# Kernel tuning notes

Hardware: AMD Instinct MI355X
Metric: run time of the kernel (lower is better)

The kernel has to match this reference:

```python
import jax, jax.numpy as jnp
import numpy as np

HEADS = 6
EPS = 1e-5


def _na_idx(L, k, d):
    # NATTEN-style dilated neighborhood: work within dilation cosets,
    # clamp window to stay inside the image (window shifts at borders).
    i = np.arange(L)
    g = i % d
    p = i // d
    Lg = (L - g + d - 1) // d  # coset length per position
    start = np.clip(p - k // 2, 0, Lg - k)
    j = np.arange(k)
    nbr = g[:, None] + d * (start[:, None] + j[None, :])          # [L,k] neighbor coords
    rel = (start[:, None] + j[None, :]) - p[:, None] + (k - 1)    # [L,k] rpb index in [0,2k-2]
    return jnp.asarray(nbr, jnp.int32), jnp.asarray(rel, jnp.int32)


def _na2d(x, qkv_w, qkv_b, proj_w, proj_b, rpb, heads, k, d):
    # x: [B,H,W,C] NHWC neighborhood attention with relative positional bias
    B, H, W, C = x.shape
    dh = C // heads
    scale = dh ** -0.5
    qkv = (x @ qkv_w + qkv_b).reshape(B, H, W, 3, heads, dh)
    qkv = jnp.transpose(qkv, (3, 0, 4, 1, 2, 5))  # [3,B,h,H,W,dh]
    q, kk, v = qkv[0] * scale, qkv[1], qkv[2]
    nh, rh = _na_idx(H, k, d)
    nw, rw = _na_idx(W, k, d)

    def gather(t):  # [B,h,H,W,dh] -> [B,h,H,W,k,k,dh]
        t = t[:, :, nh]              # [B,h,H,k,W,dh]
        t = t[:, :, :, :, nw]        # [B,h,H,k,W,k,dh]
        return jnp.transpose(t, (0, 1, 2, 4, 3, 5, 6))

    kn, vn = gather(kk), gather(v)
    attn = jnp.einsum('bhxyd,bhxyijd->bhxyij', q, kn)  # [B,h,H,W,k,k]
    bias = rpb[:, rh]                  # [h,H,k,2k-1]
    bias = bias[:, :, :, rw]           # [h,H,k,W,k]
    bias = jnp.transpose(bias, (0, 1, 3, 2, 4))  # [h,H,W,k,k]
    attn = attn + bias[None]
    attn = jax.nn.softmax(attn.reshape(B, heads, H, W, k * k), axis=-1)
    attn = attn.reshape(B, heads, H, W, k, k)
    out = jnp.einsum('bhxyij,bhxyijd->bhxyd', attn, vn)
    out = jnp.transpose(out, (0, 2, 3, 1, 4)).reshape(B, H, W, C)
    return out @ proj_w + proj_b


def _rln(x, w, b, m1_w, m1_b, m2_w, m2_b):
    # Revised LayerNorm: normalize over (C,H,W) per sample; meta1/meta2 are 1x1 convs on std/mean
    mean = jnp.mean(x, axis=(1, 2, 3), keepdims=True)
    std = jnp.sqrt(jnp.mean((x - mean) ** 2, axis=(1, 2, 3), keepdims=True) + EPS)
    out = (x - mean) / std * w + b
    rescale = m1_w[None, :, None, None] * std + m1_b[None, :, None, None]
    rebias = m2_w[None, :, None, None] * mean + m2_b[None, :, None, None]
    return out, rescale, rebias


def _c11(x, w, b):  # 1x1 conv on NCHW == per-pixel linear
    return jnp.einsum('bchw,oc->bohw', x, w) + b[None, :, None, None]


def _gelu(x):
    return jax.nn.gelu(x, approximate=False)


def reference(x, ln_w, ln_b, m1_w, m1_b, m2_w, m2_b, qkv1_w, qkv1_b, proj1_w, proj1_b, rpb1, qkv2_w, qkv2_b, proj2_w, proj2_b, rpb2, mlp_w1, mlp_b1, mlp_w2, mlp_b2, bn_g, bn_b, bn_m, bn_v, pa_w1, pa_b1, pa_w2, pa_b2, ca_w1, ca_b1, ca_w2, ca_b2, m2a_w1, m2a_b1, m2a_w2, m2a_b2):
    # ---- NA block 1 (kernel 7, dilation 1) ----
    sc = x
    y, rs, rb = _rln(x, ln_w, ln_b, m1_w, m1_b, m2_w, m2_b)
    a = _na2d(jnp.transpose(y, (0, 2, 3, 1)), qkv1_w, qkv1_b, proj1_w, proj1_b, rpb1, HEADS, 7, 1)
    x = sc + jnp.transpose(a, (0, 3, 1, 2)) * rs + rb
    # ---- NA block 2 (kernel 5, dilation 8) ----
    sc = x
    y, rs, rb = _rln(x, ln_w, ln_b, m1_w, m1_b, m2_w, m2_b)
    a = _na2d(jnp.transpose(y, (0, 2, 3, 1)), qkv2_w, qkv2_b, proj2_w, proj2_b, rpb2, HEADS, 5, 8)
    x = sc + jnp.transpose(a, (0, 3, 1, 2)) * rs + rb
    # ---- MLP (source reuses the pre-attn2 shortcut `sc`) ----
    y, rs, rb = _rln(x, ln_w, ln_b, m1_w, m1_b, m2_w, m2_b)
    m = _c11(jax.nn.relu(_c11(y, mlp_w1, mlp_b1)), mlp_w2, mlp_b2)
    x = sc + m * rs + rb
    # ---- BN + pixel attention + channel attention + mlp2 ----
    sc = x
    inv = jax.lax.rsqrt(bn_v + EPS)
    y = (x - bn_m[None, :, None, None]) * (inv * bn_g)[None, :, None, None] + bn_b[None, :, None, None]
    pa = jax.nn.sigmoid(_c11(_gelu(_c11(y, pa_w1, pa_b1)), pa_w2, pa_b2))  # [B,1,H,W]
    y = pa * y
    gap = jnp.mean(y, axis=(2, 3), keepdims=True)
    ca = jax.nn.sigmoid(_c11(_gelu(_c11(gap, ca_w1, ca_b1)), ca_w2, ca_b2))  # [B,C,1,1]
    y = ca * y
    y = _c11(_gelu(_c11(y, m2a_w1, m2a_b1)), m2a_w2, m2a_b2)
    return sc + y


def setup_inputs() -> dict:
    key = jax.random.key(0)
    B, C, H, W, HID = 4, 96, 64, 64, 384
    ks = iter(jax.random.split(key, 48))

    def rn(shape, s=0.02):
        return jax.random.normal(next(ks), shape, jnp.float32) * s

    d = {}
    d['x'] = jax.random.normal(next(ks), (B, C, H, W), jnp.float32)
    d['ln_w'] = jnp.ones((1, C, 1, 1), jnp.float32)
    d['ln_b'] = jnp.zeros((1, C, 1, 1), jnp.float32)
    d['m1_w'] = rn((C,)); d['m1_b'] = jnp.ones((C,), jnp.float32)
    d['m2_w'] = rn((C,)); d['m2_b'] = jnp.zeros((C,), jnp.float32)
    d['qkv1_w'] = rn((C, 3 * C)); d['qkv1_b'] = jnp.zeros((3 * C,), jnp.float32)
    d['proj1_w'] = rn((C, C)); d['proj1_b'] = jnp.zeros((C,), jnp.float32)
    d['rpb1'] = rn((HEADS, 13, 13))
    d['qkv2_w'] = rn((C, 3 * C)); d['qkv2_b'] = jnp.zeros((3 * C,), jnp.float32)
    d['proj2_w'] = rn((C, C)); d['proj2_b'] = jnp.zeros((C,), jnp.float32)
    d['rpb2'] = rn((HEADS, 9, 9))
    d['mlp_w1'] = rn((HID, C)); d['mlp_b1'] = jnp.zeros((HID,), jnp.float32)
    d['mlp_w2'] = rn((C, HID)); d['mlp_b2'] = jnp.zeros((C,), jnp.float32)
    d['bn_g'] = jnp.ones((C,), jnp.float32); d['bn_b'] = jnp.zeros((C,), jnp.float32)
    d['bn_m'] = jnp.zeros((C,), jnp.float32); d['bn_v'] = jnp.ones((C,), jnp.float32)
    d['pa_w1'] = rn((C // 8, C)); d['pa_b1'] = jnp.zeros((C // 8,), jnp.float32)
    d['pa_w2'] = rn((1, C // 8)); d['pa_b2'] = jnp.zeros((1,), jnp.float32)
    d['ca_w1'] = rn((C, C)); d['ca_b1'] = jnp.zeros((C,), jnp.float32)
    d['ca_w2'] = rn((C, C)); d['ca_b2'] = jnp.zeros((C,), jnp.float32)
    d['m2a_w1'] = rn((C, C)); d['m2a_b1'] = jnp.zeros((C,), jnp.float32)
    d['m2a_w2'] = rn((C, C)); d['m2a_b2'] = jnp.zeros((C,), jnp.float32)
    return d
```

## Files before the change

kernel.cpp:

```cpp
#include <hip/hip_runtime.h>
#include <math.h>

#define CC 96
#define NP 4096
#define NHEADS 6
#define NELEMF 393216.0f
#define EPSF 1e-5f

typedef __attribute__((ext_vector_type(8))) short bf16x8;
typedef __attribute__((ext_vector_type(4))) float f32x4;
#define MFMA16(a,b,c) __builtin_amdgcn_mfma_f32_16x16x32_bf16(a,b,c,0,0,0)

#define WS_STATS 0
#define WQKV1  64
#define WQKV2  (WQKV1+13824)
#define WPROJ1 (WQKV2+13824)
#define WPROJ2 (WPROJ1+4608)
#define WMLP1  (WPROJ2+4608)
#define WMLP2  (WMLP1+18432)
#define WM2A1  (WMLP2+18432)
#define WM2A2  (WM2A1+4608)
#define WPA1T  (WM2A2+4608)
#define WBNS   (WPA1T+1152)
#define WS_YPM 84352
#define WS_Q   870784
#define WS_K   (WS_Q+1572864)
#define WS_V   (WS_K+1572864)
#define WS_ATTPM (WS_V+1572864)
#define WS_X1  (WS_ATTPM+786432)
#define WS_X2  (WS_X1+1572864)
#define WS_X3  (WS_X2+1572864)
#define WS_PA  (WS_X3+1572864)
#define WS_GAP (WS_PA+16384)
#define WS_CA  (WS_GAP+384)

__device__ __forceinline__ float gelu_f(float x){
  return 0.5f * x * (1.0f + erff(x * 0.7071067811865476f));
}
__device__ __forceinline__ float sigmoid_f(float x){
  return 1.0f / (1.0f + __expf(-x));
}
__device__ __forceinline__ unsigned short bfr(float f){
  unsigned int u = __float_as_uint(f);
  u += 0x7fffu + ((u >> 16) & 1u);
  return (unsigned short)(u >> 16);
}
__device__ __forceinline__ unsigned int bfpack(float a, float b){
  return (unsigned int)bfr(a) | ((unsigned int)bfr(b) << 16);
}
__device__ __forceinline__ void get_ms(const float* st, int b, float& mean, float& inv, float& stdv){
  float s = st[b], s2 = st[4+b];
  mean = s * (1.0f/NELEMF);
  float var = fmaxf(s2 * (1.0f/NELEMF) - mean*mean, 0.0f);
  stdv = sqrtf(var + EPSF);
  inv = 1.0f / stdv;
}

__global__ void stats_kernel(const float* __restrict__ src, float* __restrict__ st){
  int b = blockIdx.x / CC, c = blockIdx.x % CC;
  const float* p = src + (b*CC + c)*NP;
  float s = 0.f, s2 = 0.f;
  for(int i = threadIdx.x; i < NP; i += 256){ float v = p[i]; s += v; s2 = fmaf(v, v, s2); }
  for(int off = 32; off > 0; off >>= 1){ s += __shfl_down(s, off); s2 += __shfl_down(s2, off); }
  __shared__ float ls[8];
  int wid = threadIdx.x >> 6;
  if((threadIdx.x & 63) == 0){ ls[wid] = s; ls[4+wid] = s2; }
  __syncthreads();
  if(threadIdx.x == 0){
    atomicAdd(&st[b],   ls[0]+ls[1]+ls[2]+ls[3]);
    atomicAdd(&st[4+b], ls[4]+ls[5]+ls[6]+ls[7]);
  }
}

__global__ void prep_weights(const float* __restrict__ q1, const float* __restrict__ q2,
                             const float* __restrict__ p1, const float* __restrict__ p2,
                             const float* __restrict__ w1, const float* __restrict__ w2,
                             const float* __restrict__ a1, const float* __restrict__ a2,
                             const float* __restrict__ pw1,
                             const float* __restrict__ bg, const float* __restrict__ bb,
                             const float* __restrict__ bm, const float* __restrict__ bv,
                             float* __restrict__ ws){
  int gid = blockIdx.x*256 + threadIdx.x;
  if(gid < 27648){ int n = gid/96, c = gid%96; ((unsigned short*)(ws+WQKV1))[gid] = bfr(q1[c*288+n]); }
  else if(gid < 55296){ int g = gid-27648; int n = g/96, c = g%96; ((unsigned short*)(ws+WQKV2))[g] = bfr(q2[c*288+n]); }
  else if(gid < 64512){ int g = gid-55296; int n = g/96, c = g%96; ((unsigned short*)(ws+WPROJ1))[g] = bfr(p1[c*96+n]); }
  else if(gid < 73728){ int g = gid-64512; int n = g/96, c = g%96; ((unsigned short*)(ws+WPROJ2))[g] = bfr(p2[c*96+n]); }
  else if(gid < 110592){ int g = gid-73728; ((unsigned short*)(ws+WMLP1))[g] = bfr(w1[g]); }
  else if(gid < 147456){ int g = gid-110592; ((unsigned short*)(ws+WMLP2))[g] = bfr(w2[g]); }
  else if(gid < 156672){ int g = gid-147456; ((unsigned short*)(ws+WM2A1))[g] = bfr(a1[g]); }
  else if(gid < 165888){ int g = gid-156672; ((unsigned short*)(ws+WM2A2))[g] = bfr(a2[g]); }
  else if(gid < 167040){ int g = gid-165888; int c = g/12, h = g%12; ws[WPA1T + g] = pw1[h*96+c]; }
  else if(gid < 167136){ int c = gid-167040;
    float sc = rsqrtf(bv[c] + EPSF) * bg[c];
    ws[WBNS + c] = sc;
    ws[WBNS + 96 + c] = bb[c] - bm[c]*sc;
  }
}

__global__ void __launch_bounds__(256) ln_tr_kernel(
    const float* __restrict__ src, const float* __restrict__ st,
    const float* __restrict__ lnw, const float* __restrict__ lnb,
    unsigned int* __restrict__ dst){
  int px0 = blockIdx.x*64; int b = px0 >> 12; int pxl0 = px0 & 4095;
  float mean, inv, stdv; get_ms(st, b, mean, inv, stdv);
  __shared__ float T[96*67];
  for(int idx = threadIdx.x; idx < 96*64; idx += 256){
    int c = idx >> 6, p = idx & 63;
    float s = inv*lnw[c]; float o = lnb[c] - mean*s;
    T[c*67 + p] = fmaf(src[(b*96 + c)*NP + pxl0 + p], s, o);
  }
  __syncthreads();
  for(int idx = threadIdx.x; idx < 64*48; idx += 256){
    int row = idx/48, cd = idx%48;
    dst[(px0 + row)*48 + cd] = bfpack(T[(2*cd)*67 + row], T[(2*cd+1)*67 + row]);
  }
}

__global__ void __launch_bounds__(256) y3_tr_kernel(
    const float* __restrict__ x3, const float* __restrict__ bns,
    const float* __restrict__ pa, const float* __restrict__ ca,
    unsigned int* __restrict__ dst){
  int px0 = blockIdx.x*64; int b = px0 >> 12; int pxl0 = px0 & 4095;
  __shared__ float T[96*67];
  for(int idx = threadIdx.x; idx < 96*64; idx += 256){
    int c = idx >> 6, p = idx & 63;
    float v = fmaf(x3[(b*96 + c)*NP + pxl0 + p], bns[c], bns[96 + c]);
    T[c*67 + p] = v * ca[b*96 + c] * pa[px0 + p];
  }
  __syncthreads();
  for(int idx = threadIdx.x; idx < 64*48; idx += 256){
    int row = idx/48, cd = idx%48;
    dst[(px0 + row)*48 + cd] = bfpack(T[(2*cd)*67 + row], T[(2*cd+1)*67 + row]);
  }
}

template<int K>
__device__ __forceinline__ void mfma_tile(const unsigned short* __restrict__ A,
                                          const unsigned short* __restrict__ W,
                                          int m_base, int n_base, f32x4 acc[2][3]){
  int lane = threadIdx.x & 63;
  int ml = lane & 15, q = lane >> 4;
  const bf16x8* a0 = (const bf16x8*)(A + (size_t)(m_base + ml)*K + q*8);
  const bf16x8* a1 = (const bf16x8*)(A + (size_t)(m_base + 16 + ml)*K + q*8);
  const bf16x8* b0 = (const bf16x8*)(W + (n_base + ml)*K + q*8);
  const bf16x8* b1 = (const bf16x8*)(W + (n_base + 16 + ml)*K + q*8);
  const bf16x8* b2 = (const bf16x8*)(W + (n_base + 32 + ml)*K + q*8);
  #pragma unroll
  for(int ks = 0; ks < K/32; ++ks){
    bf16x8 av0 = a0[ks*4], av1 = a1[ks*4];
    bf16x8 bv0 = b0[ks*4], bv1 = b1[ks*4], bv2 = b2[ks*4];
    acc[0][0] = MFMA16(av0, bv0, acc[0][0]);
    acc[0][1] = MFMA16(av0, bv1, acc[0][1]);
    acc[0][2] = MFMA16(av0, bv2, acc[0][2]);
    acc[1][0] = MFMA16(av1, bv0, acc[1][0]);
    acc[1][1] = MFMA16(av1, bv1, acc[1][1]);
    acc[1][2] = MFMA16(av1, bv2, acc[1][2]);
  }
}

__global__ void __launch_bounds__(256) gemm_qkv_kernel(
    const unsigned short* __restrict__ ypm, const unsigned short* __restrict__ wT,
    const float* __restrict__ qb,
    float* __restrict__ qo, float* __restrict__ ko, float* __restrict__ vo){
  int w = threadIdx.x >> 6, lane = threadIdx.x & 63;
  int ml = lane & 15, q = lane >> 4;
  int m_base = blockIdx.x*128 + w*32;
  int n0 = blockIdx.y*48;
  f32x4 acc[2][3];
  f32x4 z = {0.f,0.f,0.f,0.f};
  #pragma unroll
  for(int f=0; f<2; ++f) for(int g=0; g<3; ++g) acc[f][g] = z;
  mfma_tile<96>(ypm, wT, m_base, n0, acc);
  #pragma unroll
  for(int g = 0; g < 3; ++g){
    int nfb = n0 + g*16;
    int t = nfb/96, head = (nfb%96) >> 4;
    float scale = (t == 0) ? 0.25f : 1.0f;
    float* dst = (t == 0) ? qo : (t == 1) ? ko : vo;
    float bias = qb[nfb + ml];
    #pragma unroll
    for(int f = 0; f < 2; ++f){
      #pragma unroll
      for(int r = 0; r < 4; ++r){
        int m = m_base + f*16 + q*4 + r;
        int b = m >> 12, pxl = m & 4095;
        dst[(((size_t)(b*NHEADS + head))*NP + pxl)*16 + ml] = (acc[f][g][r] + bias)*scale;
      }
    }
  }
}

__global__ void __launch_bounds__(256) gemm_proj_kernel(
    const unsigned short* __restrict__ attpm, const unsigned short* __restrict__ wT,
    const float* __restrict__ pb, const float* __restrict__ scx, const float* __restrict__ st,
    const float* __restrict__ m1w, const float* __restrict__ m1b,
    const float* __restrict__ m2w, const float* __restrict__ m2b,
    float* __restrict__ dst, float* __restrict__ st_out){
  int w = threadIdx.x >> 6, lane = threadIdx.x & 63;
  int ml = lane & 15, q = lane >> 4;
  int m_base = blockIdx.x*128 + w*32;
  int n0 = blockIdx.y*48;
  f32x4 acc[2][3];
  f32x4 z = {0.f,0.f,0.f,0.f};
  #pragma unroll
  for(int f=0; f<2; ++f) for(int g=0; g<3; ++g) acc[f][g] = z;
  mfma_tile<96>(attpm, wT, m_base, n0, acc);
  __shared__ float T[48*133];
  #pragma unroll
  for(int f = 0; f < 2; ++f)
    #pragma unroll
    for(int g = 0; g < 3; ++g)
      #pragma unroll
      for(int r = 0; r < 4; ++r)
        T[(g*16 + ml)*133 + w*32 + f*16 + q*4 + r] = acc[f][g][r];
  __syncthreads();
  int b = (blockIdx.x*128) >> 12, pxl0 = (blockIdx.x*128) & 4095;
  float mean, inv, stdv; get_ms(st, b, mean, inv, stdv);
  float s = 0.f, s2 = 0.f;
  for(int idx = threadIdx.x; idx < 48*128; idx += 256){
    int row = idx >> 7, px = idx & 127;
    int n = n0 + row;
    float rsf = fmaf(m1w[n], stdv, m1b[n]);
    float rbf = fmaf(m2w[n], mean, m2b[n]);
    int ad = (b*CC + n)*NP + pxl0 + px;
    float val = scx[ad] + (T[row*133 + px] + pb[n])*rsf + rbf;
    dst[ad] = val;
    s += val; s2 = fmaf(val, val, s2);
  }
  for(int off = 32; off > 0; off >>= 1){ s += __shfl_down(s, off); s2 += __shfl_down(s2, off); }
  __shared__ float ls[8];
  int wid = threadIdx.x >> 6;
  if((threadIdx.x & 63) == 0){ ls[wid] = s; ls[4+wid] = s2; }
  __syncthreads();
  if(threadIdx.x == 0){
    atomicAdd(&st_out[b],   ls[0]+ls[1]+ls[2]+ls[3]);
    atomicAdd(&st_out[4+b], ls[4]+ls[5]+ls[6]+ls[7]);
  }
}

__global__ void __launch_bounds__(256) gemm_mlp1_kernel(
    const unsigned short* __restrict__ ypm, const unsigned short* __restrict__ wT,
    const float* __restrict__ b1, unsigned short* __restrict__ hid){
  int w = threadIdx.x >> 6, lane = threadIdx.x & 63;
  int ml = lane & 15, q = lane >> 4;
  int m_base = blockIdx.x*128 + w*32;
  int n0 = blockIdx.y*48;
  f32x4 acc[2][3];
  f32x4 z = {0.f,0.f,0.f,0.f};
  #pragma unroll
  for(int f=0; f<2; ++f) for(int g=0; g<3; ++g) acc[f][g] = z;
  mfma_tile<96>(ypm, wT, m_base, n0, acc);
  #pragma unroll
  for(int g = 0; g < 3; ++g){
    int n = n0 + g*16 + ml;
    float bias = b1[n];
    #pragma unroll
    for(int f = 0; f < 2; ++f)
      #pragma unroll
      for(int r = 0; r < 4; ++r){
        int m = m_base + f*16 + q*4 + r;
        hid[(size_t)m*384 + n] = bfr(fmaxf(acc[f][g][r] + bias, 0.f));
      }
  }
}

__global__ void __launch_bounds__(256) gemm_mlp2_kernel(
    const unsigned short* __restrict__ hid, const unsigned short* __restrict__ wT,
    const float* __restrict__ b2, const float* __restrict__ scx, const float* __restrict__ st,
    const float* __restrict__ m1w, const float* __restrict__ m1b,
    const float* __restrict__ m2w, const float* __restrict__ m2b,
    float* __restrict__ dst){
  int w = threadIdx.x >> 6, lane = threadIdx.x & 63;
  int ml = lane & 15, q = lane >> 4;
  int m_base = blockIdx.x*128 + w*32;
  int n0 = blockIdx.y*48;
  f32x4 acc[2][3];
  f32x4 z = {0.f,0.f,0.f,0.f};
  #pragma unroll
  for(int f=0; f<2; ++f) for(int g=0; g<3; ++g) acc[f][g] = z;
  mfma_tile<384>(hid, wT, m_base, n0, acc);
  __shared__ float T[48*133];
  #pragma unroll
  for(int f = 0; f < 2; ++f)
    #pragma unroll
    for(int g = 0; g < 3; ++g)
      #pragma unroll
      for(int r = 0; r < 4; ++r)
        T[(g*16 + ml)*133 + w*32 + f*16 + q*4 + r] = acc[f][g][r];
  __syncthreads();
  int b = (blockIdx.x*128) >> 12, pxl0 = (blockIdx.x*128) & 4095;
  float mean, inv, stdv; get_ms(st, b, mean, inv, stdv);
  for(int idx = threadIdx.x; idx < 48*128; idx += 256){
    int row = idx >> 7, px = idx & 127;
    int n = n0 + row;
    float rsf = fmaf(m1w[n], stdv, m1b[n]);
    float rbf = fmaf(m2w[n], mean, m2b[n]);
    int ad = (b*CC + n)*NP + pxl0 + px;
    dst[ad] = scx[ad] + (T[row*133 + px] + b2[n])*rsf + rbf;
  }
}

__global__ void __launch_bounds__(256) gemm_m2a1_kernel(
    const unsigned short* __restrict__ y3pm, const unsigned short* __restrict__ wT,
    const float* __restrict__ b1, unsigned short* __restrict__ tpm){
  int w = threadIdx.x >> 6, lane = threadIdx.x & 63;
  int ml = lane & 15, q = lane >> 4;
  int m_base = blockIdx.x*128 + w*32;
  int n0 = blockIdx.y*48;
  f32x4 acc[2][3];
  f32x4 z = {0.f,0.f,0.f,0.f};
  #pragma unroll
  for(int f=0; f<2; ++f) for(int g=0; g<3; ++g) acc[f][g] = z;
  mfma_tile<96>(y3pm, wT, m_base, n0, acc);
  #pragma unroll
  for(int g = 0; g < 3; ++g){
    int n = n0 + g*16 + ml;
    float bias = b1[n];
    #pragma unroll
    for(int f = 0; f < 2; ++f)
      #pragma unroll
      for(int r = 0; r < 4; ++r){
        int m = m_base + f*16 + q*4 + r;
        tpm[(size_t)m*96 + n] = bfr(gelu_f(acc[f][g][r] + bias));
      }
  }
}

__global__ void __launch_bounds__(256) gemm_m2a2_kernel(
    const unsigned short* __restrict__ tpm, const unsigned short* __restrict__ wT,
    const float* __restrict__ b2, const float* __restrict__ scx, float* __restrict__ outp){
  int w = threadIdx.x >> 6, lane = threadIdx.x & 63;
  int ml = lane & 15, q = lane >> 4;
  int m_base = blockIdx.x*128 + w*32;
  int n0 = blockIdx.y*48;
  f32x4 acc[2][3];
  f32x4 z = {0.f,0.f,0.f,0.f};
  #pragma unroll
  for(int f=0; f<2; ++f) for(int g=0; g<3; ++g) acc[f][g] = z;
  mfma_tile<96>(tpm, wT, m_base, n0, acc);
  __shared__ float T[48*133];
  #pragma unroll
  for(int f = 0; f < 2; ++f)
    #pragma unroll
    for(int g = 0; g < 3; ++g)
      #pragma unroll
      for(int r = 0; r < 4; ++r)
        T[(g*16 + ml)*133 + w*32 + f*16 + q*4 + r] = acc[f][g][r];
  __syncthreads();
  int b = (blockIdx.x*128) >> 12, pxl0 = (blockIdx.x*128) & 4095;
  for(int idx = threadIdx.x; idx < 48*128; idx += 256){
    int row = idx >> 7, px = idx & 127;
    int n = n0 + row;
    int ad = (b*CC + n)*NP + pxl0 + px;
    outp[ad] = scx[ad] + T[row*133 + px] + b2[n];
  }
}

template<int K, int D, int RPB>
__global__ void __launch_bounds__(256) attn_kernel(
    const float* __restrict__ qb, const float* __restrict__ kb,
    const float* __restrict__ vb, const float* __restrict__ rpb,
    unsigned short* __restrict__ outp){
  int bh = blockIdx.x >> 6;
  int x = blockIdx.x & 63;
  int head = bh % NHEADS, b = bh / NHEADS;

  int gx = x % D, px = x / D;
  int Lgx = (64 - gx + D - 1) / D;
  int sx = min(max(px - K/2, 0), Lgx - K);

  __shared__ float sm[2*K*1024];
  float* kl = sm;
  float* vl = sm + K*1024;
  const float* kg = kb + (size_t)bh*NP*16;
  const float* vg = vb + (size_t)bh*NP*16;
  int tid = threadIdx.x;
  #pragma unroll
  for(int i = 0; i < K; ++i){
    int hh = gx + D*(sx + i);
    ((float4*)(kl + i*1024))[tid] = ((const float4*)(kg + hh*1024))[tid];
    ((float4*)(vl + i*1024))[tid] = ((const float4*)(vg + hh*1024))[tid];
  }
  __syncthreads();

  int pixoff = tid >> 2, t = tid & 3;
  int y = pixoff;
  int pix = x*64 + y;
  const float4 q = *(const float4*)(qb + ((size_t)bh*NP + pix)*16 + 4*t);

  int gy = y % D, py = y / D;
  int Lgy = (64 - gy + D - 1) / D;
  int sy = min(max(py - K/2, 0), Lgy - K);

  float sc[K*K];
  #pragma unroll
  for(int i = 0; i < K; ++i){
    #pragma unroll
    for(int j = 0; j < K; ++j){
      int ww = gy + D*(sy + j);
      float4 kv = *(const float4*)(kl + i*1024 + ww*16 + 4*t);
      float s = q.x*kv.x;
      s = fmaf(q.y, kv.y, s); s = fmaf(q.z, kv.z, s); s = fmaf(q.w, kv.w, s);
      sc[i*K + j] = s;
    }
  }
  float mx = -1e30f;
  #pragma unroll
  for(int i = 0; i < K; ++i){
    const float* brow = rpb + (head*RPB + (sx + i - px + (K-1)))*RPB + (sy - py + (K-1));
    #pragma unroll
    for(int j = 0; j < K; ++j){
      float s = sc[i*K + j];
      s += __shfl_xor(s, 1);
      s += __shfl_xor(s, 2);
      s += brow[j];
      sc[i*K + j] = s;
      mx = fmaxf(mx, s);
    }
  }
  float sum = 0.f;
  #pragma unroll
  for(int n = 0; n < K*K; ++n){ float e = __expf(sc[n] - mx); sc[n] = e; sum += e; }
  float rs = 1.0f / sum;
  float4 acc = {0,0,0,0};
  #pragma unroll
  for(int i = 0; i < K; ++i){
    #pragma unroll
    for(int j = 0; j < K; ++j){
      int ww = gy + D*(sy + j);
      float wgt = sc[i*K + j] * rs;
      float4 vv = *(const float4*)(vl + i*1024 + ww*16 + 4*t);
      acc.x = fmaf(wgt, vv.x, acc.x); acc.y = fmaf(wgt, vv.y, acc.y);
      acc.z = fmaf(wgt, vv.z, acc.z); acc.w = fmaf(wgt, vv.w, acc.w);
    }
  }
  ushort4 o4;
  o4.x = bfr(acc.x); o4.y = bfr(acc.y); o4.z = bfr(acc.z); o4.w = bfr(acc.w);
  *(ushort4*)(outp + ((size_t)(b*NP + pix))*96 + head*16 + 4*t) = o4;
}

__global__ void __launch_bounds__(64) pa_kernel(
    const float* __restrict__ x3, const float* __restrict__ bns,
    const float* __restrict__ w1t, const float* __restrict__ b1,
    const float* __restrict__ w2, const float* __restrict__ b2,
    float* __restrict__ pa){
  int pix = blockIdx.x*64 + threadIdx.x;
  int b = blockIdx.x >> 6;
  int p = pix & 4095;
  float acc[12];
  #pragma unroll
  for(int h = 0; h < 12; ++h) acc[h] = b1[h];
  #pragma unroll 4
  for(int c = 0; c < CC; ++c){
    float yv = fmaf(x3[(b*CC + c)*NP + p], bns[c], bns[96 + c]);
    #pragma unroll
    for(int h = 0; h < 12; ++h) acc[h] = fmaf(yv, w1t[c*12 + h], acc[h]);
  }
  float s = b2[0];
  #pragma unroll
  for(int h = 0; h < 12; ++h) s = fmaf(gelu_f(acc[h]), w2[h], s);
  pa[pix] = sigmoid_f(s);
}

__global__ void gap_kernel(const float* __restrict__ x3, const float* __restrict__ bns,
                           const float* __restrict__ pa, float* __restrict__ gap){
  int b = blockIdx.x / CC, c = blockIdx.x % CC;
  float scb = bns[c], shb = bns[96 + c];
  float s = 0.f;
  for(int i = threadIdx.x; i < NP; i += 256)
    s = fmaf(fmaf(x3[(b*CC + c)*NP + i], scb, shb), pa[b*NP + i], s);
  for(int off = 32; off > 0; off >>= 1) s += __shfl_down(s, off);
  __shared__ float ls[4];
  if((threadIdx.x & 63) == 0) ls[threadIdx.x >> 6] = s;
  __syncthreads();
  if(threadIdx.x == 0) gap[blockIdx.x] = (ls[0]+ls[1]+ls[2]+ls[3]) * (1.0f/4096.0f);
}

__global__ void ca_kernel(const float* __restrict__ gap, const float* __restrict__ w1,
                          const float* __restrict__ b1, const float* __restrict__ w2,
                          const float* __restrict__ b2, float* __restrict__ ca){
  int b = blockIdx.x; int o = threadIdx.x;
  __shared__ float g[96], t[96];
  if(o < 96) g[o] = gap[b*96 + o];
  __syncthreads();
  if(o < 96){
    float a = b1[o];
    for(int c = 0; c < 96; ++c) a = fmaf(g[c], w1[o*96 + c], a);
    t[o] = gelu_f(a);
  }
  __syncthreads();
  if(o < 96){
    float a = b2[o];
    for(int c = 0; c < 96; ++c) a = fmaf(t[c], w2[o*96 + c], a);
    ca[b*96 + o] = sigmoid_f(a);
  }
}

extern "C" void kernel_launch(void* const* d_in, const int* in_sizes, int n_in,
                              void* d_out, int out_size, void* d_ws, size_t ws_size,
                              hipStream_t stream){
  (void)in_sizes; (void)n_in; (void)out_size; (void)ws_size;
  const float* x     = (const float*)d_in[0];
  const float* lnw   = (const float*)d_in[1];
  const float* lnb   = (const float*)d_in[2];
  const float* m1w   = (const float*)d_in[3];
  const float* m1b   = (const float*)d_in[4];
  const float* m2w   = (const float*)d_in[5];
  const float* m2b   = (const float*)d_in[6];
  const float* qkv1w = (const float*)d_in[7];
  const float* qkv1b = (const float*)d_in[8];
  const float* proj1w= (const float*)d_in[9];
  const float* proj1b= (const float*)d_in[10];
  const float* rpb1  = (const float*)d_in[11];
  const float* qkv2w = (const float*)d_in[12];
  const float* qkv2b = (const float*)d_in[13];
  const float* proj2w= (const float*)d_in[14];
  const float* proj2b= (const float*)d_in[15];
  const float* rpb2  = (const float*)d_in[16];
  const float* mw1   = (const float*)d_in[17];
  const float* mb1   = (const float*)d_in[18];
  const float* mw2   = (const float*)d_in[19];
  const float* mb2   = (const float*)d_in[20];
  const float* bng   = (const float*)d_in[21];
  const float* bnb   = (const float*)d_in[22];
  const float* bnm   = (const float*)d_in[23];
  const float* bnv   = (const float*)d_in[24];
  const float* paw1  = (const float*)d_in[25];
  const float* pab1  = (const float*)d_in[26];
  const float* paw2  = (const float*)d_in[27];
  const float* pab2  = (const float*)d_in[28];
  const float* caw1  = (const float*)d_in[29];
  const float* cab1  = (const float*)d_in[30];
  const float* caw2  = (const float*)d_in[31];
  const float* cab2  = (const float*)d_in[32];
  const float* aw1   = (const float*)d_in[33];
  const float* ab1   = (const float*)d_in[34];
  const float* aw2   = (const float*)d_in[35];
  const float* ab2   = (const float*)d_in[36];

  float* ws  = (float*)d_ws;
  float* out = (float*)d_out;
  float* st0 = ws + WS_STATS;
  float* st1 = st0 + 8;
  float* st2 = st0 + 16;
  unsigned short* ypm   = (unsigned short*)(ws + WS_YPM);
  float* q   = ws + WS_Q;
  float* k   = ws + WS_K;
  float* v   = ws + WS_V;
  unsigned short* attpm = (unsigned short*)(ws + WS_ATTPM);
  unsigned short* hid   = (unsigned short*)(ws + WS_Q);
  unsigned short* tpm   = (unsigned short*)(ws + WS_Q);
  float* x1  = ws + WS_X1;
  float* x2  = ws + WS_X2;
  float* x3  = ws + WS_X3;
  float* pab = ws + WS_PA;
  float* gpb = ws + WS_GAP;
  float* cab = ws + WS_CA;
  float* bns = ws + WBNS;

  hipMemsetAsync(d_ws, 0, 64*sizeof(float), stream);
  prep_weights<<<653, 256, 0, stream>>>(qkv1w, qkv2w, proj1w, proj2w, mw1, mw2, aw1, aw2,
                                        paw1, bng, bnb, bnm, bnv, ws);

  stats_kernel<<<384, 256, 0, stream>>>(x, st0);
  ln_tr_kernel<<<256, 256, 0, stream>>>(x, st0, lnw, lnb, (unsigned int*)ypm);
  gemm_qkv_kernel<<<dim3(128,6), 256, 0, stream>>>(ypm, (unsigned short*)(ws+WQKV1), qkv1b, q, k, v);
  attn_kernel<7,1,13><<<1536, 256, 0, stream>>>(q, k, v, rpb1, attpm);
  gemm_proj_kernel<<<dim3(128,2), 256, 0, stream>>>(attpm, (unsigned short*)(ws+WPROJ1), proj1b,
                                                    x, st0, m1w, m1b, m2w, m2b, x1, st1);

  ln_tr_kernel<<<256, 256, 0, stream>>>(x1, st1, lnw, lnb, (unsigned int*)ypm);
  gemm_qkv_kernel<<<dim3(128,6), 256, 0, stream>>>(ypm, (unsigned short*)(ws+WQKV2), qkv2b, q, k, v);
  attn_kernel<5,8,9><<<1536, 256, 0, stream>>>(q, k, v, rpb2, attpm);
  gemm_proj_kernel<<<dim3(128,2), 256, 0, stream>>>(attpm, (unsigned short*)(ws+WPROJ2), proj2b,
                                                    x1, st1, m1w, m1b, m2w, m2b, x2, st2);

  ln_tr_kernel<<<256, 256, 0, stream>>>(x2, st2, lnw, lnb, (unsigned int*)ypm);
  gemm_mlp1_kernel<<<dim3(128,8), 256, 0, stream>>>(ypm, (unsigned short*)(ws+WMLP1), mb1, hid);
  gemm_mlp2_kernel<<<dim3(128,2), 256, 0, stream>>>(hid, (unsigned short*)(ws+WMLP2), mb2,
                                                    x1, st2, m1w, m1b, m2w, m2b, x3);

  pa_kernel<<<256, 64, 0, stream>>>(x3, bns, ws + WPA1T, pab1, paw2, pab2, pab);
  gap_kernel<<<384, 256, 0, stream>>>(x3, bns, pab, gpb);
  ca_kernel<<<4, 128, 0, stream>>>(gpb, caw1, cab1, caw2, cab2, cab);
  y3_tr_kernel<<<256, 256, 0, stream>>>(x3, bns, pab, cab, (unsigned int*)ypm);
  gemm_m2a1_kernel<<<dim3(128,2), 256, 0, stream>>>(ypm, (unsigned short*)(ws+WM2A1), ab1, tpm);
  gemm_m2a2_kernel<<<dim3(128,2), 256, 0, stream>>>(tpm, (unsigned short*)(ws+WM2A2), ab2, x3, out);
}
```

Measured before the change: 307.3 us.

## Store Q/K/V in bf16, fuse m2a GEMM pair, reshape pa launch

Q, K and V are now written as bf16 by the QKV GEMM, and the attention kernel loads bf16 into half-size shared memory, unpacking to fp32 for the dot products. This halves the attention's global and LDS traffic, at the cost of lower-precision Q/K/V. The two m2a GEMMs are fused into one kernel that keeps the GELU hidden tile in shared memory, removing a launch and a global round trip. The pa kernel moves from 256 blocks of 64 threads to 64 blocks of 256 threads and unrolls its channel loop more.

```diff
diff --git a/kernel.cpp b/kernel.cpp
--- a/kernel.cpp
+++ b/kernel.cpp
@@ -24,9 +24,9 @@
 #define WBNS   (WPA1T+1152)
 #define WS_YPM 84352
 #define WS_Q   870784
-#define WS_K   (WS_Q+1572864)
-#define WS_V   (WS_K+1572864)
-#define WS_ATTPM (WS_V+1572864)
+#define WS_K   (WS_Q+786432)
+#define WS_V   (WS_K+786432)
+#define WS_ATTPM (WS_V+786432)
 #define WS_X1  (WS_ATTPM+786432)
 #define WS_X2  (WS_X1+1572864)
 #define WS_X3  (WS_X2+1572864)
@@ -48,6 +48,8 @@
 __device__ __forceinline__ unsigned int bfpack(float a, float b){
   return (unsigned int)bfr(a) | ((unsigned int)bfr(b) << 16);
 }
+__device__ __forceinline__ float bflo(unsigned int u){ return __uint_as_float(u << 16); }
+__device__ __forceinline__ float bfhi(unsigned int u){ return __uint_as_float(u & 0xffff0000u); }
 __device__ __forceinline__ void get_ms(const float* st, int b, float& mean, float& inv, float& stdv){
   float s = st[b], s2 = st[4+b];
   mean = s * (1.0f/NELEMF);
@@ -161,7 +163,7 @@
 __global__ void __launch_bounds__(256) gemm_qkv_kernel(
     const unsigned short* __restrict__ ypm, const unsigned short* __restrict__ wT,
     const float* __restrict__ qb,
-    float* __restrict__ qo, float* __restrict__ ko, float* __restrict__ vo){
+    unsigned short* __restrict__ qo, unsigned short* __restrict__ ko, unsigned short* __restrict__ vo){
   int w = threadIdx.x >> 6, lane = threadIdx.x & 63;
   int ml = lane & 15, q = lane >> 4;
   int m_base = blockIdx.x*128 + w*32;
@@ -176,7 +178,7 @@
     int nfb = n0 + g*16;
     int t = nfb/96, head = (nfb%96) >> 4;
     float scale = (t == 0) ? 0.25f : 1.0f;
-    float* dst = (t == 0) ? qo : (t == 1) ? ko : vo;
+    unsigned short* dst = (t == 0) ? qo : (t == 1) ? ko : vo;
     float bias = qb[nfb + ml];
     #pragma unroll
     for(int f = 0; f < 2; ++f){
@@ -184,7 +186,7 @@
       for(int r = 0; r < 4; ++r){
         int m = m_base + f*16 + q*4 + r;
         int b = m >> 12, pxl = m & 4095;
-        dst[(((size_t)(b*NHEADS + head))*NP + pxl)*16 + ml] = (acc[f][g][r] + bias)*scale;
+        dst[(((size_t)(b*NHEADS + head))*NP + pxl)*16 + ml] = bfr((acc[f][g][r] + bias)*scale);
       }
     }
   }
@@ -300,66 +302,88 @@
   }
 }
 
-__global__ void __launch_bounds__(256) gemm_m2a1_kernel(
-    const unsigned short* __restrict__ y3pm, const unsigned short* __restrict__ wT,
-    const float* __restrict__ b1, unsigned short* __restrict__ tpm){
+__global__ void __launch_bounds__(256) gemm_m2a_kernel(
+    const unsigned short* __restrict__ y3pm,
+    const unsigned short* __restrict__ w1T, const float* __restrict__ b1,
+    const unsigned short* __restrict__ w2T, const float* __restrict__ b2,
+    const float* __restrict__ scx, float* __restrict__ outp){
+  __shared__ __align__(16) char smbuf[128*104*2];
+  unsigned short* tl = (unsigned short*)smbuf;
+  float* T = (float*)smbuf;
   int w = threadIdx.x >> 6, lane = threadIdx.x & 63;
   int ml = lane & 15, q = lane >> 4;
   int m_base = blockIdx.x*128 + w*32;
-  int n0 = blockIdx.y*48;
-  f32x4 acc[2][3];
   f32x4 z = {0.f,0.f,0.f,0.f};
-  #pragma unroll
-  for(int f=0; f<2; ++f) for(int g=0; g<3; ++g) acc[f][g] = z;
-  mfma_tile<96>(y3pm, wT, m_base, n0, acc);
-  #pragma unroll
-  for(int g = 0; g < 3; ++g){
-    int n = n0 + g*16 + ml;
-    float bias = b1[n];
+  f32x4 acc[2][6];
+  #pragma unroll
+  for(int f=0; f<2; ++f) for(int g=0; g<6; ++g) acc[f][g] = z;
+  {
+    const bf16x8* a0 = (const bf16x8*)(y3pm + (size_t)(m_base + ml)*96 + q*8);
+    const bf16x8* a1 = (const bf16x8*)(y3pm + (size_t)(m_base + 16 + ml)*96 + q*8);
+    #pragma unroll
+    for(int ks = 0; ks < 3; ++ks){
+      bf16x8 av0 = a0[ks*4], av1 = a1[ks*4];
+      #pragma unroll
+      for(int g = 0; g < 6; ++g){
+        bf16x8 bv = *(const bf16x8*)(w1T + (g*16 + ml)*96 + ks*32 + q*8);
+        acc[0][g] = MFMA16(av0, bv, acc[0][g]);
+        acc[1][g] = MFMA16(av1, bv, acc[1][g]);
+      }
+    }
+  }
+  #pragma unroll
+  for(int g = 0; g < 6; ++g){
+    float bias = b1[g*16 + ml];
     #pragma unroll
     for(int f = 0; f < 2; ++f)
       #pragma unroll
-      for(int r = 0; r < 4; ++r){
-        int m = m_base + f*16 + q*4 + r;
-        tpm[(size_t)m*96 + n] = bfr(gelu_f(acc[f][g][r] + bias));
+      for(int r = 0; r < 4; ++r)
+        tl[(w*32 + f*16 + q*4 + r)*104 + g*16 + ml] = bfr(gelu_f(acc[f][g][r] + bias));
+  }
+  __syncthreads();
+  f32x4 acc2[2][6];
+  #pragma unroll
+  for(int f=0; f<2; ++f) for(int g=0; g<6; ++g) acc2[f][g] = z;
+  {
+    const unsigned short* ar0 = tl + (w*32 + ml)*104;
+    const unsigned short* ar1 = tl + (w*32 + 16 + ml)*104;
+    #pragma unroll
+    for(int ks = 0; ks < 3; ++ks){
+      bf16x8 av0 = *(const bf16x8*)(ar0 + ks*32 + q*8);
+      bf16x8 av1 = *(const bf16x8*)(ar1 + ks*32 + q*8);
+      #pragma unroll
+      for(int g = 0; g < 6; ++g){
+        bf16x8 bv = *(const bf16x8*)(w2T + (g*16 + ml)*96 + ks*32 + q*8);
+        acc2[0][g] = MFMA16(av0, bv, acc2[0][g]);
+        acc2[1][g] = MFMA16(av1, bv, acc2[1][g]);
       }
-  }
-}
-
-__global__ void __launch_bounds__(256) gemm_m2a2_kernel(
-    const unsigned short* __restrict__ tpm, const unsigned short* __restrict__ wT,
-    const float* __restrict__ b2, const float* __restrict__ scx, float* __restrict__ outp){
-  int w = threadIdx.x >> 6, lane = threadIdx.x & 63;
-  int ml = lane & 15, q = lane >> 4;
-  int m_base = blockIdx.x*128 + w*32;
-  int n0 = blockIdx.y*48;
-  f32x4 acc[2][3];
-  f32x4 z = {0.f,0.f,0.f,0.f};
-  #pragma unroll
-  for(int f=0; f<2; ++f) for(int g=0; g<3; ++g) acc[f][g] = z;
-  mfma_tile<96>(tpm, wT, m_base, n0, acc);
-  __shared__ float T[48*133];
-  #pragma unroll
-  for(int f = 0; f < 2; ++f)
-    #pragma unroll
-    for(int g = 0; g < 3; ++g)
-      #pragma unroll
-      for(int r = 0; r < 4; ++r)
-        T[(g*16 + ml)*133 + w*32 + f*16 + q*4 + r] = acc[f][g][r];
-  __syncthreads();
+    }
+  }
   int b = (blockIdx.x*128) >> 12, pxl0 = (blockIdx.x*128) & 4095;
-  for(int idx = threadIdx.x; idx < 48*128; idx += 256){
-    int row = idx >> 7, px = idx & 127;
-    int n = n0 + row;
-    int ad = (b*CC + n)*NP + pxl0 + px;
-    outp[ad] = scx[ad] + T[row*133 + px] + b2[n];
+  #pragma unroll
+  for(int half = 0; half < 2; ++half){
+    __syncthreads();
+    #pragma unroll
+    for(int f = 0; f < 2; ++f)
+      #pragma unroll
+      for(int g = 0; g < 3; ++g)
+        #pragma unroll
+        for(int r = 0; r < 4; ++r)
+          T[(g*16 + ml)*133 + w*32 + f*16 + q*4 + r] = acc2[f][half*3 + g][r];
+    __syncthreads();
+    for(int idx = threadIdx.x; idx < 48*128; idx += 256){
+      int row = idx >> 7, px = idx & 127;
+      int n = half*48 + row;
+      int ad = (b*CC + n)*NP + pxl0 + px;
+      outp[ad] = scx[ad] + T[row*133 + px] + b2[n];
+    }
   }
 }
 
 template<int K, int D, int RPB>
 __global__ void __launch_bounds__(256) attn_kernel(
-    const float* __restrict__ qb, const float* __restrict__ kb,
-    const float* __restrict__ vb, const float* __restrict__ rpb,
+    const unsigned short* __restrict__ qb, const unsigned short* __restrict__ kb,
+    const unsigned short* __restrict__ vb, const float* __restrict__ rpb,
     unsigned short* __restrict__ outp){
   int bh = blockIdx.x >> 6;
   int x = blockIdx.x & 63;
@@ -369,24 +393,25 @@
   int Lgx = (64 - gx + D - 1) / D;
   int sx = min(max(px - K/2, 0), Lgx - K);
 
-  __shared__ float sm[2*K*1024];
-  float* kl = sm;
-  float* vl = sm + K*1024;
-  const float* kg = kb + (size_t)bh*NP*16;
-  const float* vg = vb + (size_t)bh*NP*16;
+  __shared__ unsigned int sm[2*K*512];
+  unsigned int* kl = sm;
+  unsigned int* vl = sm + K*512;
+  const unsigned int* kg = (const unsigned int*)(kb + (size_t)bh*NP*16);
+  const unsigned int* vg = (const unsigned int*)(vb + (size_t)bh*NP*16);
   int tid = threadIdx.x;
   #pragma unroll
   for(int i = 0; i < K; ++i){
     int hh = gx + D*(sx + i);
-    ((float4*)(kl + i*1024))[tid] = ((const float4*)(kg + hh*1024))[tid];
-    ((float4*)(vl + i*1024))[tid] = ((const float4*)(vg + hh*1024))[tid];
+    ((uint2*)(kl + i*512))[tid] = ((const uint2*)(kg + hh*512))[tid];
+    ((uint2*)(vl + i*512))[tid] = ((const uint2*)(vg + hh*512))[tid];
   }
   __syncthreads();
 
   int pixoff = tid >> 2, t = tid & 3;
   int y = pixoff;
   int pix = x*64 + y;
-  const float4 q = *(const float4*)(qb + ((size_t)bh*NP + pix)*16 + 4*t);
+  uint2 qd = *(const uint2*)(qb + ((size_t)bh*NP + pix)*16 + 4*t);
+  float qx = bflo(qd.x), qy = bfhi(qd.x), qz = bflo(qd.y), qw = bfhi(qd.y);
 
   int gy = y % D, py = y / D;
   int Lgy = (64 - gy + D - 1) / D;
@@ -398,9 +423,11 @@
     #pragma unroll
     for(int j = 0; j < K; ++j){
       int ww = gy + D*(sy + j);
-      float4 kv = *(const float4*)(kl + i*1024 + ww*16 + 4*t);
-      float s = q.x*kv.x;
-      s = fmaf(q.y, kv.y, s); s = fmaf(q.z, kv.z, s); s = fmaf(q.w, kv.w, s);
+      uint2 kv = *(const uint2*)(kl + i*512 + ww*8 + t*2);
+      float s = qx*bflo(kv.x);
+      s = fmaf(qy, bfhi(kv.x), s);
+      s = fmaf(qz, bflo(kv.y), s);
+      s = fmaf(qw, bfhi(kv.y), s);
       sc[i*K + j] = s;
     }
   }
@@ -429,9 +456,11 @@
     for(int j = 0; j < K; ++j){
       int ww = gy + D*(sy + j);
       float wgt = sc[i*K + j] * rs;
-      float4 vv = *(const float4*)(vl + i*1024 + ww*16 + 4*t);
-      acc.x = fmaf(wgt, vv.x, acc.x); acc.y = fmaf(wgt, vv.y, acc.y);
-      acc.z = fmaf(wgt, vv.z, acc.z); acc.w = fmaf(wgt, vv.w, acc.w);
+      uint2 vv = *(const uint2*)(vl + i*512 + ww*8 + t*2);
+      acc.x = fmaf(wgt, bflo(vv.x), acc.x);
+      acc.y = fmaf(wgt, bfhi(vv.x), acc.y);
+      acc.z = fmaf(wgt, bflo(vv.y), acc.z);
+      acc.w = fmaf(wgt, bfhi(vv.y), acc.w);
     }
   }
   ushort4 o4;
@@ -439,18 +468,17 @@
   *(ushort4*)(outp + ((size_t)(b*NP + pix))*96 + head*16 + 4*t) = o4;
 }
 
-__global__ void __launch_bounds__(64) pa_kernel(
+__global__ void __launch_bounds__(256) pa_kernel(
     const float* __restrict__ x3, const float* __restrict__ bns,
     const float* __restrict__ w1t, const float* __restrict__ b1,
     const float* __restrict__ w2, const float* __restrict__ b2,
     float* __restrict__ pa){
-  int pix = blockIdx.x*64 + threadIdx.x;
-  int b = blockIdx.x >> 6;
-  int p = pix & 4095;
+  int b = blockIdx.x >> 4;
+  int p = (blockIdx.x & 15)*256 + threadIdx.x;
   float acc[12];
   #pragma unroll
   for(int h = 0; h < 12; ++h) acc[h] = b1[h];
-  #pragma unroll 4
+  #pragma unroll 8
   for(int c = 0; c < CC; ++c){
     float yv = fmaf(x3[(b*CC + c)*NP + p], bns[c], bns[96 + c]);
     #pragma unroll
@@ -459,7 +487,7 @@
   float s = b2[0];
   #pragma unroll
   for(int h = 0; h < 12; ++h) s = fmaf(gelu_f(acc[h]), w2[h], s);
-  pa[pix] = sigmoid_f(s);
+  pa[b*NP + p] = sigmoid_f(s);
 }
 
 __global__ void gap_kernel(const float* __restrict__ x3, const float* __restrict__ bns,
@@ -544,12 +572,11 @@
   float* st1 = st0 + 8;
   float* st2 = st0 + 16;
   unsigned short* ypm   = (unsigned short*)(ws + WS_YPM);
-  float* q   = ws + WS_Q;
-  float* k   = ws + WS_K;
-  float* v   = ws + WS_V;
+  unsigned short* q     = (unsigned short*)(ws + WS_Q);
+  unsigned short* k     = (unsigned short*)(ws + WS_K);
+  unsigned short* v     = (unsigned short*)(ws + WS_V);
   unsigned short* attpm = (unsigned short*)(ws + WS_ATTPM);
   unsigned short* hid   = (unsigned short*)(ws + WS_Q);
-  unsigned short* tpm   = (unsigned short*)(ws + WS_Q);
   float* x1  = ws + WS_X1;
   float* x2  = ws + WS_X2;
   float* x3  = ws + WS_X3;
@@ -580,10 +607,10 @@
   gemm_mlp2_kernel<<<dim3(128,2), 256, 0, stream>>>(hid, (unsigned short*)(ws+WMLP2), mb2,
                                                     x1, st2, m1w, m1b, m2w, m2b, x3);
 
-  pa_kernel<<<256, 64, 0, stream>>>(x3, bns, ws + WPA1T, pab1, paw2, pab2, pab);
+  pa_kernel<<<64, 256, 0, stream>>>(x3, bns, ws + WPA1T, pab1, paw2, pab2, pab);
   gap_kernel<<<384, 256, 0, stream>>>(x3, bns, pab, gpb);
   ca_kernel<<<4, 128, 0, stream>>>(gpb, caw1, cab1, caw2, cab2, cab);
   y3_tr_kernel<<<256, 256, 0, stream>>>(x3, bns, pab, cab, (unsigned int*)ypm);
-  gemm_m2a1_kernel<<<dim3(128,2), 256, 0, stream>>>(ypm, (unsigned short*)(ws+WM2A1), ab1, tpm);
-  gemm_m2a2_kernel<<<dim3(128,2), 256, 0, stream>>>(tpm, (unsigned short*)(ws+WM2A2), ab2, x3, out);
-}
+  gemm_m2a_kernel<<<128, 256, 0, stream>>>(ypm, (unsigned short*)(ws+WM2A1), ab1,
+                                           (unsigned short*)(ws+WM2A2), ab2, x3, out);
+}
```

New measurement: 305.5 us. No clear change (-0.6%).
